# Performance work log

Hardware: AMD Instinct MI355X
Metric: run time of the kernel (lower is better)

## Reference

```python
import jax, jax.numpy as jnp
import numpy as np

B, L = 64, 1024
ENC_DIM, DEC_DIM, ATT_DIM = 512, 512, 512


def setup_inputs() -> dict:
    key = jax.random.key(0)
    ks = jax.random.split(key, 11)
    s_enc = 1.0 / np.sqrt(ENC_DIM)
    s_dec = 1.0 / np.sqrt(DEC_DIM)
    s_att = 1.0 / np.sqrt(ATT_DIM)
    return {
        "encoder_features": jax.random.normal(ks[0], (B, L, ENC_DIM), jnp.float32),
        "decoder_hidden": jax.random.normal(ks[1], (B, DEC_DIM), jnp.float32),
        "coverage": jax.random.uniform(ks[2], (B, L), jnp.float32),
        # nn.Linear params (torch stores weight as [out, in]; we keep [in, out])
        "W_enc": jax.random.uniform(ks[3], (ENC_DIM, ATT_DIM), jnp.float32, -s_enc, s_enc),
        "b_enc": jax.random.uniform(ks[4], (ATT_DIM,), jnp.float32, -s_enc, s_enc),
        "W_dec": jax.random.uniform(ks[5], (DEC_DIM, ATT_DIM), jnp.float32, -s_dec, s_dec),
        "b_dec": jax.random.uniform(ks[6], (ATT_DIM,), jnp.float32, -s_dec, s_dec),
        "W_cov": jax.random.uniform(ks[7], (1, ATT_DIM), jnp.float32, -1.0, 1.0),
        "b_cov": jax.random.uniform(ks[8], (ATT_DIM,), jnp.float32, -1.0, 1.0),
        "W_full": jax.random.uniform(ks[9], (ATT_DIM, 1), jnp.float32, -s_att, s_att),
        "b_full": jax.random.uniform(ks[10], (1,), jnp.float32, -s_att, s_att),
    }


def reference(encoder_features, decoder_hidden, coverage,
              W_enc, b_enc, W_dec, b_dec, W_cov, b_cov, W_full, b_full):
    # att1: [B, L, A]
    att1 = jnp.einsum("ble,ea->bla", encoder_features, W_enc) + b_enc
    # att2: [B, 1, A]
    att2 = (decoder_hidden @ W_dec + b_dec)[:, None, :]
    # att3: coverage[B,L] through Linear(1, A) -> outer product, [B, L, A]
    att3 = coverage[:, :, None] * W_cov[0] + b_cov
    # energy: [B, L]
    energy = (jax.nn.relu(att1 + att2 + att3) @ W_full)[:, :, 0] + b_full[0]
    alpha = jax.nn.softmax(energy, axis=1)  # [B, L]
    new_coverage = coverage + alpha
    attention_weighted_encoding = jnp.einsum("ble,bl->be", encoder_features, alpha)
    return (attention_weighted_encoding, alpha, new_coverage)
```

## Files before the change

kernel.cpp:

```cpp
#include <hip/hip_runtime.h>
#include <cstdint>
#include <cstddef>

#define NB   64
#define NL   1024
#define NA   512
#define NE   512

typedef __attribute__((ext_vector_type(8))) short bf16x8;
typedef __attribute__((ext_vector_type(4))) float f32x4;

__device__ __forceinline__ unsigned short f2bf(float x){
    unsigned int u = __float_as_uint(x);
    u += 0x7FFFu + ((u >> 16) & 1u);
    return (unsigned short)(u >> 16);
}

__global__ __launch_bounds__(256) void k_prep(const float* __restrict__ Wenc,
                                              unsigned short* __restrict__ wfrag,
                                              const float* __restrict__ dh,
                                              const float* __restrict__ Wdec,
                                              const float* __restrict__ bdec,
                                              const float* __restrict__ benc,
                                              const float* __restrict__ bcov,
                                              float* __restrict__ base){
    const int bid = blockIdx.x, tid = threadIdx.x;
    if (bid < 128){
        const int g    = bid * 256 + tid;
        const int lane = g & 63;
        const int n    = (g >> 6) & 3;
        const int ks   = (g >> 8) & 1;
        const int cw   = (g >> 9) & 7;
        const int s    = g >> 12;
        const int col  = cw * 64 + n * 16 + (lane & 15);
        const int kb   = s * 64 + ks * 32 + (lane >> 4) * 8;
        unsigned int w[4];
        #pragma unroll
        for (int p = 0; p < 4; ++p){
            unsigned short lo = f2bf(Wenc[(size_t)(kb + 2*p    ) * NA + col]);
            unsigned short hi = f2bf(Wenc[(size_t)(kb + 2*p + 1) * NA + col]);
            w[p] = (unsigned int)lo | ((unsigned int)hi << 16);
        }
        ((uint4*)wfrag)[g] = make_uint4(w[0], w[1], w[2], w[3]);
    } else {
        const int idx = bid - 128;
        const int b   = idx >> 3;
        const int a0  = (idx & 7) * 64;
        const int al  = tid & 63, kg = tid >> 6;
        __shared__ float h[512];
        __shared__ float ps[4][64];
        h[tid]       = dh[b * 512 + tid];
        h[tid + 256] = dh[b * 512 + tid + 256];
        __syncthreads();
        const float* wp = Wdec + (size_t)(kg * 128) * 512 + a0 + al;
        const float* hp = h + kg * 128;
        float s0 = 0.f, s1 = 0.f, s2 = 0.f, s3 = 0.f;
        #pragma unroll
        for (int k = 0; k < 128; k += 4){
            s0 += hp[k + 0] * wp[(size_t)(k + 0) * 512];
            s1 += hp[k + 1] * wp[(size_t)(k + 1) * 512];
            s2 += hp[k + 2] * wp[(size_t)(k + 2) * 512];
            s3 += hp[k + 3] * wp[(size_t)(k + 3) * 512];
        }
        ps[kg][al] = (s0 + s1) + (s2 + s3);
        __syncthreads();
        if (tid < 64){
            const int a = a0 + tid;
            base[b * 512 + a] = ps[0][tid] + ps[1][tid] + ps[2][tid] + ps[3][tid]
                              + bdec[a] + benc[a] + bcov[a];
        }
    }
}

__global__ __launch_bounds__(256, 2) void k_energy(
        const float* __restrict__ enc,
        const float* __restrict__ cov,
        const float* __restrict__ base,
        const unsigned short* __restrict__ wfrag,
        const float* __restrict__ Wcov,
        const float* __restrict__ Wfull,
        float* __restrict__ energy)
{
    __shared__ __align__(16) unsigned char sB[65536];
    __shared__ __align__(16) unsigned char sA[8192];
    __shared__ float sCov[64];
    __shared__ float sEp[4][64];

    const int tid  = threadIdx.x;
    const int wid  = tid >> 6, lane = tid & 63;
    const int r0   = blockIdx.x * 64;
    const int b    = r0 >> 10;

    if (tid < 64) sCov[tid] = cov[r0 + tid];

    f32x4 acc[4][8];
    #pragma unroll
    for (int m = 0; m < 4; ++m)
        #pragma unroll
        for (int n = 0; n < 8; ++n) acc[m][n] = (f32x4){0.f, 0.f, 0.f, 0.f};

    const int rloc = tid >> 2, q = tid & 3;
    const float* arow = enc + (size_t)(r0 + rloc) * NE + q * 16;
    unsigned char* aw = sA + (((q >> 1) * 4 + (rloc >> 4)) * 1024
                              + ((rloc & 15) + 32 * (q & 1)) * 16);
    const unsigned char* bsrc = (const unsigned char*)wfrag + wid * 16384 + lane * 16;
    unsigned char* bdst = sB + wid * 16384;

    for (int s = 0; s < 8; ++s){
        __syncthreads();
        const unsigned char* bs = bsrc + (size_t)s * 65536;
        #pragma unroll
        for (int i = 0; i < 16; ++i){
            __builtin_amdgcn_global_load_lds(
                (__attribute__((address_space(1))) void*)(bs + i * 1024),
                (__attribute__((address_space(3))) void*)(bdst + i * 1024),
                16, 0, 0);
        }
        const float* ap = arow + s * 64;
        float4 v0 = *(const float4*)(ap);
        float4 v1 = *(const float4*)(ap + 4);
        float4 v2 = *(const float4*)(ap + 8);
        float4 v3 = *(const float4*)(ap + 12);
        uint4 f1, f2;
        f1.x = f2bf(v0.x) | ((unsigned)f2bf(v0.y) << 16);
        f1.y = f2bf(v0.z) | ((unsigned)f2bf(v0.w) << 16);
        f1.z = f2bf(v1.x) | ((unsigned)f2bf(v1.y) << 16);
        f1.w = f2bf(v1.z) | ((unsigned)f2bf(v1.w) << 16);
        f2.x = f2bf(v2.x) | ((unsigned)f2bf(v2.y) << 16);
        f2.y = f2bf(v2.z) | ((unsigned)f2bf(v2.w) << 16);
        f2.z = f2bf(v3.x) | ((unsigned)f2bf(v3.y) << 16);
        f2.w = f2bf(v3.z) | ((unsigned)f2bf(v3.w) << 16);
        *(uint4*)(aw)       = f1;
        *(uint4*)(aw + 256) = f2;
        __syncthreads();
        bf16x8 af[2][4];
        #pragma unroll
        for (int ks = 0; ks < 2; ++ks)
            #pragma unroll
            for (int m = 0; m < 4; ++m)
                af[ks][m] = *(const bf16x8*)(sA + (ks*4 + m) * 1024 + lane * 16);
        #pragma unroll
        for (int ks = 0; ks < 2; ++ks){
            #pragma unroll
            for (int n = 0; n < 8; ++n){
                bf16x8 bfr = *(const bf16x8*)(sB
                    + ((wid*2 + (n>>2)) * 512 + ks * 256 + (n&3) * 64 + lane) * 16);
                #pragma unroll
                for (int m = 0; m < 4; ++m)
                    acc[m][n] = __builtin_amdgcn_mfma_f32_16x16x32_bf16(
                                    af[ks][m], bfr, acc[m][n], 0, 0, 0);
            }
        }
    }

    const int c0 = wid * 128 + (lane & 15);
    float basev[8], wcovv[8], wfullv[8];
    #pragma unroll
    for (int n = 0; n < 8; ++n){
        const int c = c0 + ((n >> 2) * 64) + (n & 3) * 16;
        basev[n]  = base[b * 512 + c];
        wcovv[n]  = Wcov[c];
        wfullv[n] = Wfull[c];
    }
    const int hi = lane >> 4;
    float covr[4][4];
    #pragma unroll
    for (int m = 0; m < 4; ++m)
        #pragma unroll
        for (int r = 0; r < 4; ++r) covr[m][r] = sCov[m*16 + 4*hi + r];
    float epv[4][4] = {};
    #pragma unroll
    for (int m = 0; m < 4; ++m)
        #pragma unroll
        for (int n = 0; n < 8; ++n)
            #pragma unroll
            for (int r = 0; r < 4; ++r){
                float v = acc[m][n][r] + basev[n] + covr[m][r] * wcovv[n];
                v = fmaxf(v, 0.f);
                epv[m][r] += v * wfullv[n];
            }
    #pragma unroll
    for (int m = 0; m < 4; ++m)
        #pragma unroll
        for (int r = 0; r < 4; ++r){
            float v = epv[m][r];
            v += __shfl_xor(v, 1);
            v += __shfl_xor(v, 2);
            v += __shfl_xor(v, 4);
            v += __shfl_xor(v, 8);
            epv[m][r] = v;
        }
    if ((lane & 15) == 0){
        #pragma unroll
        for (int m = 0; m < 4; ++m)
            #pragma unroll
            for (int r = 0; r < 4; ++r)
                sEp[wid][m*16 + 4*hi + r] = epv[m][r];
    }
    __syncthreads();
    if (tid < 64)
        energy[r0 + tid] = sEp[0][tid] + sEp[1][tid] + sEp[2][tid] + sEp[3][tid];
}

#define AWE_OFF   0
#define ALPHA_OFF 32768
#define NCOV_OFF  98304

__global__ __launch_bounds__(256) void k_finish(
        const float* __restrict__ enc, const float* __restrict__ cov,
        const float* __restrict__ energy, float* __restrict__ out)
{
    const int bid = blockIdx.x;
    const int b = bid >> 3, ec = bid & 7;
    const int tid = threadIdx.x;
    __shared__ float sa[1024];
    __shared__ float rb[16];
    __shared__ float ps2[16][64];

    float4 ev = ((const float4*)(energy + b * 1024))[tid];
    float mx = fmaxf(fmaxf(ev.x, ev.y), fmaxf(ev.z, ev.w));
    #pragma unroll
    for (int off = 32; off; off >>= 1) mx = fmaxf(mx, __shfl_xor(mx, off));
    if ((tid & 63) == 0) rb[tid >> 6] = mx;
    __syncthreads();
    mx = fmaxf(fmaxf(rb[0], rb[1]), fmaxf(rb[2], rb[3]));
    float e0 = __expf(ev.x - mx), e1 = __expf(ev.y - mx),
          e2 = __expf(ev.z - mx), e3 = __expf(ev.w - mx);
    ((float4*)sa)[tid] = make_float4(e0, e1, e2, e3);
    float sm = e0 + e1 + e2 + e3;
    #pragma unroll
    for (int off = 32; off; off >>= 1) sm += __shfl_xor(sm, off);
    if ((tid & 63) == 0) rb[8 + (tid >> 6)] = sm;
    __syncthreads();
    const float inv = 1.0f / (rb[8] + rb[9] + rb[10] + rb[11]);

    if (ec == 0){
        #pragma unroll
        for (int i = 0; i < 4; ++i){
            const int idx = tid + i * 256;
            const float a = sa[idx] * inv;
            out[ALPHA_OFF + b * 1024 + idx] = a;
            out[NCOV_OFF  + b * 1024 + idx] = cov[b * 1024 + idx] + a;
        }
    }

    const int cg = tid & 15, rg = tid >> 4;
    const float4* ep = (const float4*)(enc + (size_t)(b * 1024 + rg * 64) * 512)
                     + ec * 16 + cg;
    const float* w = sa + rg * 64;
    float ax = 0.f, ay = 0.f, az = 0.f, aw = 0.f;
    #pragma unroll 8
    for (int l = 0; l < 64; ++l){
        float4 e4 = ep[(size_t)l * 128];
        const float wl = w[l];
        ax += e4.x * wl; ay += e4.y * wl; az += e4.z * wl; aw += e4.w * wl;
    }
    ps2[rg][cg * 4 + 0] = ax;
    ps2[rg][cg * 4 + 1] = ay;
    ps2[rg][cg * 4 + 2] = az;
    ps2[rg][cg * 4 + 3] = aw;
    __syncthreads();
    if (tid < 64){
        float s = 0.f;
        #pragma unroll
        for (int g = 0; g < 16; ++g) s += ps2[g][tid];
        out[AWE_OFF + b * 512 + ec * 64 + tid] = s * inv;
    }
}

extern "C" void kernel_launch(void* const* d_in, const int* in_sizes, int n_in,
                              void* d_out, int out_size, void* d_ws, size_t ws_size,
                              hipStream_t stream){
    const float* enc   = (const float*)d_in[0];
    const float* dh    = (const float*)d_in[1];
    const float* cov   = (const float*)d_in[2];
    const float* Wenc  = (const float*)d_in[3];
    const float* benc  = (const float*)d_in[4];
    const float* Wdec  = (const float*)d_in[5];
    const float* bdec  = (const float*)d_in[6];
    const float* Wcov  = (const float*)d_in[7];
    const float* bcov  = (const float*)d_in[8];
    const float* Wfull = (const float*)d_in[9];
    float* out = (float*)d_out;

    unsigned short* wfrag = (unsigned short*)d_ws;
    float* base   = (float*)((char*)d_ws + 512 * 1024);
    float* energy = (float*)((char*)d_ws + 640 * 1024);

    k_prep  <<<640,  256, 0, stream>>>(Wenc, wfrag, dh, Wdec, bdec, benc, bcov, base);
    k_energy<<<1024, 256, 0, stream>>>(enc, cov, base, wfrag, Wcov, Wfull, energy);
    k_finish<<<512,  256, 0, stream>>>(enc, cov, energy, out);
}
```

Before: 82.07 us.

## Load MFMA operands directly from global memory, dropping LDS staging

The energy GEMM kernel no longer stages the bf16 weight fragments and the converted encoder tile through shared memory. Each wave now reads its B fragments and its fp32 A rows straight from global memory into registers, converting to bf16 in place, which removes the per-step barriers and the 72KB of LDS. The cost is that every wave re-reads the same A rows (four waves share them), and global-load latency now sits directly in front of the MFMAs with no double buffering.

```diff
diff --git a/kernel.cpp b/kernel.cpp
--- a/kernel.cpp
+++ b/kernel.cpp
@@ -9,6 +9,9 @@
 
 typedef __attribute__((ext_vector_type(8))) short bf16x8;
 typedef __attribute__((ext_vector_type(4))) float f32x4;
+typedef __attribute__((ext_vector_type(4))) unsigned int u32x4;
+
+union PackU { u32x4 u; bf16x8 h; };
 
 __device__ __forceinline__ unsigned short f2bf(float x){
     unsigned int u = __float_as_uint(x);
@@ -81,9 +84,6 @@
         const float* __restrict__ Wfull,
         float* __restrict__ energy)
 {
-    __shared__ __align__(16) unsigned char sB[65536];
-    __shared__ __align__(16) unsigned char sA[8192];
-    __shared__ float sCov[64];
     __shared__ float sEp[4][64];
 
     const int tid  = threadIdx.x;
@@ -91,93 +91,72 @@
     const int r0   = blockIdx.x * 64;
     const int b    = r0 >> 10;
 
-    if (tid < 64) sCov[tid] = cov[r0 + tid];
+    const float* aB = enc + (size_t)(r0 + (lane & 15)) * NE + 8 * (lane >> 4);
+    const bf16x8* bB = (const bf16x8*)wfrag + (wid * 2) * 512 + lane;
 
     f32x4 acc[4][8];
     #pragma unroll
     for (int m = 0; m < 4; ++m)
         #pragma unroll
-        for (int n = 0; n < 8; ++n) acc[m][n] = (f32x4){0.f, 0.f, 0.f, 0.f};
-
-    const int rloc = tid >> 2, q = tid & 3;
-    const float* arow = enc + (size_t)(r0 + rloc) * NE + q * 16;
-    unsigned char* aw = sA + (((q >> 1) * 4 + (rloc >> 4)) * 1024
-                              + ((rloc & 15) + 32 * (q & 1)) * 16);
-    const unsigned char* bsrc = (const unsigned char*)wfrag + wid * 16384 + lane * 16;
-    unsigned char* bdst = sB + wid * 16384;
-
+        for (int nn = 0; nn < 8; ++nn) acc[m][nn] = (f32x4){0.f, 0.f, 0.f, 0.f};
+
+    #pragma unroll 1
     for (int s = 0; s < 8; ++s){
-        __syncthreads();
-        const unsigned char* bs = bsrc + (size_t)s * 65536;
-        #pragma unroll
-        for (int i = 0; i < 16; ++i){
-            __builtin_amdgcn_global_load_lds(
-                (__attribute__((address_space(1))) void*)(bs + i * 1024),
-                (__attribute__((address_space(3))) void*)(bdst + i * 1024),
-                16, 0, 0);
-        }
-        const float* ap = arow + s * 64;
-        float4 v0 = *(const float4*)(ap);
-        float4 v1 = *(const float4*)(ap + 4);
-        float4 v2 = *(const float4*)(ap + 8);
-        float4 v3 = *(const float4*)(ap + 12);
-        uint4 f1, f2;
-        f1.x = f2bf(v0.x) | ((unsigned)f2bf(v0.y) << 16);
-        f1.y = f2bf(v0.z) | ((unsigned)f2bf(v0.w) << 16);
-        f1.z = f2bf(v1.x) | ((unsigned)f2bf(v1.y) << 16);
-        f1.w = f2bf(v1.z) | ((unsigned)f2bf(v1.w) << 16);
-        f2.x = f2bf(v2.x) | ((unsigned)f2bf(v2.y) << 16);
-        f2.y = f2bf(v2.z) | ((unsigned)f2bf(v2.w) << 16);
-        f2.z = f2bf(v3.x) | ((unsigned)f2bf(v3.y) << 16);
-        f2.w = f2bf(v3.z) | ((unsigned)f2bf(v3.w) << 16);
-        *(uint4*)(aw)       = f1;
-        *(uint4*)(aw + 256) = f2;
-        __syncthreads();
-        bf16x8 af[2][4];
-        #pragma unroll
-        for (int ks = 0; ks < 2; ++ks)
-            #pragma unroll
-            for (int m = 0; m < 4; ++m)
-                af[ks][m] = *(const bf16x8*)(sA + (ks*4 + m) * 1024 + lane * 16);
         #pragma unroll
         for (int ks = 0; ks < 2; ++ks){
-            #pragma unroll
-            for (int n = 0; n < 8; ++n){
-                bf16x8 bfr = *(const bf16x8*)(sB
-                    + ((wid*2 + (n>>2)) * 512 + ks * 256 + (n&3) * 64 + lane) * 16);
+            bf16x8 bfr[8];
+            #pragma unroll
+            for (int nn = 0; nn < 8; ++nn)
+                bfr[nn] = bB[s * 4096 + (nn >> 2) * 512 + ks * 256 + (nn & 3) * 64];
+            bf16x8 af[4];
+            #pragma unroll
+            for (int m = 0; m < 4; ++m){
+                const float* ap = aB + (size_t)(m * 16) * NE + s * 64 + ks * 32;
+                float4 lo = *(const float4*)(ap);
+                float4 hi = *(const float4*)(ap + 4);
+                PackU u;
+                u.u = (u32x4){
+                    (unsigned)f2bf(lo.x) | ((unsigned)f2bf(lo.y) << 16),
+                    (unsigned)f2bf(lo.z) | ((unsigned)f2bf(lo.w) << 16),
+                    (unsigned)f2bf(hi.x) | ((unsigned)f2bf(hi.y) << 16),
+                    (unsigned)f2bf(hi.z) | ((unsigned)f2bf(hi.w) << 16)};
+                af[m] = u.h;
+            }
+            #pragma unroll
+            for (int nn = 0; nn < 8; ++nn)
                 #pragma unroll
                 for (int m = 0; m < 4; ++m)
-                    acc[m][n] = __builtin_amdgcn_mfma_f32_16x16x32_bf16(
-                                    af[ks][m], bfr, acc[m][n], 0, 0, 0);
-            }
+                    acc[m][nn] = __builtin_amdgcn_mfma_f32_16x16x32_bf16(
+                                    af[m], bfr[nn], acc[m][nn], 0, 0, 0);
         }
     }
 
     const int c0 = wid * 128 + (lane & 15);
     float basev[8], wcovv[8], wfullv[8];
     #pragma unroll
-    for (int n = 0; n < 8; ++n){
-        const int c = c0 + ((n >> 2) * 64) + (n & 3) * 16;
-        basev[n]  = base[b * 512 + c];
-        wcovv[n]  = Wcov[c];
-        wfullv[n] = Wfull[c];
-    }
-    const int hi = lane >> 4;
+    for (int nn = 0; nn < 8; ++nn){
+        const int c = c0 + (nn >> 2) * 64 + (nn & 3) * 16;
+        basev[nn]  = base[b * 512 + c];
+        wcovv[nn]  = Wcov[c];
+        wfullv[nn] = Wfull[c];
+    }
+    const int hi4 = lane >> 4;
     float covr[4][4];
     #pragma unroll
     for (int m = 0; m < 4; ++m)
         #pragma unroll
-        for (int r = 0; r < 4; ++r) covr[m][r] = sCov[m*16 + 4*hi + r];
+        for (int r = 0; r < 4; ++r)
+            covr[m][r] = cov[r0 + m * 16 + 4 * hi4 + r];
     float epv[4][4] = {};
     #pragma unroll
     for (int m = 0; m < 4; ++m)
         #pragma unroll
-        for (int n = 0; n < 8; ++n)
+        for (int nn = 0; nn < 8; ++nn)
             #pragma unroll
             for (int r = 0; r < 4; ++r){
-                float v = acc[m][n][r] + basev[n] + covr[m][r] * wcovv[n];
+                float v = acc[m][nn][r] + basev[nn] + covr[m][r] * wcovv[nn];
                 v = fmaxf(v, 0.f);
-                epv[m][r] += v * wfullv[n];
+                epv[m][r] += v * wfullv[nn];
             }
     #pragma unroll
     for (int m = 0; m < 4; ++m)
@@ -195,7 +174,7 @@
         for (int m = 0; m < 4; ++m)
             #pragma unroll
             for (int r = 0; r < 4; ++r)
-                sEp[wid][m*16 + 4*hi + r] = epv[m][r];
+                sEp[wid][m * 16 + 4 * hi4 + r] = epv[m][r];
     }
     __syncthreads();
     if (tid < 64)
```

After: 127.1 us. 54.8% more time.

## Double-buffer LDS tiles in energy GEMM to overlap loads with MFMA

Applied to the files above, without the earlier changes.

The energy kernel now keeps two LDS buffers each for the bf16 encoder tile and the weight-fragment tile. It prefetches the next K-slice's weights via global_load_lds and holds the raw encoder rows two slices ahead in registers, packing them into the alternate buffer after the MFMA work. This cuts the barriers per K step from two to one and overlaps global latency with compute. In exchange the LDS footprint roughly doubles to about 145KB per block, which likely allows only one block per CU instead of two, and the prefetched encoder rows add register pressure.

```diff
diff --git a/kernel.cpp b/kernel.cpp
--- a/kernel.cpp
+++ b/kernel.cpp
@@ -72,6 +72,25 @@
     }
 }
 
+#define LOAD_RAW(av, ap)                                         \
+    { av[0] = *(const float4*)(ap);                              \
+      av[1] = *(const float4*)((ap) + 4);                        \
+      av[2] = *(const float4*)((ap) + 8);                        \
+      av[3] = *(const float4*)((ap) + 12); }
+
+#define PACK_STORE(av, dst)                                      \
+    { uint4 f1, f2;                                              \
+      f1.x = f2bf(av[0].x) | ((unsigned)f2bf(av[0].y) << 16);    \
+      f1.y = f2bf(av[0].z) | ((unsigned)f2bf(av[0].w) << 16);    \
+      f1.z = f2bf(av[1].x) | ((unsigned)f2bf(av[1].y) << 16);    \
+      f1.w = f2bf(av[1].z) | ((unsigned)f2bf(av[1].w) << 16);    \
+      f2.x = f2bf(av[2].x) | ((unsigned)f2bf(av[2].y) << 16);    \
+      f2.y = f2bf(av[2].z) | ((unsigned)f2bf(av[2].w) << 16);    \
+      f2.z = f2bf(av[3].x) | ((unsigned)f2bf(av[3].y) << 16);    \
+      f2.w = f2bf(av[3].z) | ((unsigned)f2bf(av[3].w) << 16);    \
+      *(uint4*)(dst)       = f1;                                 \
+      *(uint4*)((dst)+256) = f2; }
+
 __global__ __launch_bounds__(256, 2) void k_energy(
         const float* __restrict__ enc,
         const float* __restrict__ cov,
@@ -81,8 +100,8 @@
         const float* __restrict__ Wfull,
         float* __restrict__ energy)
 {
-    __shared__ __align__(16) unsigned char sB[65536];
-    __shared__ __align__(16) unsigned char sA[8192];
+    __shared__ __align__(16) unsigned char sB[2][65536];
+    __shared__ __align__(16) unsigned char sA[2][8192];
     __shared__ float sCov[64];
     __shared__ float sEp[4][64];
 
@@ -101,49 +120,57 @@
 
     const int rloc = tid >> 2, q = tid & 3;
     const float* arow = enc + (size_t)(r0 + rloc) * NE + q * 16;
-    unsigned char* aw = sA + (((q >> 1) * 4 + (rloc >> 4)) * 1024
-                              + ((rloc & 15) + 32 * (q & 1)) * 16);
+    const int awoff = ((q >> 1) * 4 + (rloc >> 4)) * 1024
+                    + ((rloc & 15) + 32 * (q & 1)) * 16;
     const unsigned char* bsrc = (const unsigned char*)wfrag + wid * 16384 + lane * 16;
-    unsigned char* bdst = sB + wid * 16384;
-
-    for (int s = 0; s < 8; ++s){
-        __syncthreads();
-        const unsigned char* bs = bsrc + (size_t)s * 65536;
+
+    float4 avA[4], avB[4];
+
+    {
+        float4 p[4];
+        LOAD_RAW(p, arow);
+        PACK_STORE(p, sA[0] + awoff);
         #pragma unroll
         for (int i = 0; i < 16; ++i){
             __builtin_amdgcn_global_load_lds(
-                (__attribute__((address_space(1))) void*)(bs + i * 1024),
-                (__attribute__((address_space(3))) void*)(bdst + i * 1024),
+                (__attribute__((address_space(1))) void*)(bsrc + i * 1024),
+                (__attribute__((address_space(3))) void*)(sB[0] + wid * 16384 + i * 1024),
                 16, 0, 0);
         }
-        const float* ap = arow + s * 64;
-        float4 v0 = *(const float4*)(ap);
-        float4 v1 = *(const float4*)(ap + 4);
-        float4 v2 = *(const float4*)(ap + 8);
-        float4 v3 = *(const float4*)(ap + 12);
-        uint4 f1, f2;
-        f1.x = f2bf(v0.x) | ((unsigned)f2bf(v0.y) << 16);
-        f1.y = f2bf(v0.z) | ((unsigned)f2bf(v0.w) << 16);
-        f1.z = f2bf(v1.x) | ((unsigned)f2bf(v1.y) << 16);
-        f1.w = f2bf(v1.z) | ((unsigned)f2bf(v1.w) << 16);
-        f2.x = f2bf(v2.x) | ((unsigned)f2bf(v2.y) << 16);
-        f2.y = f2bf(v2.z) | ((unsigned)f2bf(v2.w) << 16);
-        f2.z = f2bf(v3.x) | ((unsigned)f2bf(v3.y) << 16);
-        f2.w = f2bf(v3.z) | ((unsigned)f2bf(v3.w) << 16);
-        *(uint4*)(aw)       = f1;
-        *(uint4*)(aw + 256) = f2;
-        __syncthreads();
+        LOAD_RAW(avB, arow + 64);
+    }
+    __syncthreads();
+
+    #pragma unroll
+    for (int s = 0; s < 8; ++s){
+        const int cb = s & 1;
+        if (s < 6){
+            const float* ap = arow + (s + 2) * 64;
+            if ((s & 1) == 0) { LOAD_RAW(avA, ap) }
+            else              { LOAD_RAW(avB, ap) }
+        }
+        if (s < 7){
+            const unsigned char* bs = bsrc + (size_t)(s + 1) * 65536;
+            unsigned char* bdst = sB[cb ^ 1] + wid * 16384;
+            #pragma unroll
+            for (int i = 0; i < 16; ++i){
+                __builtin_amdgcn_global_load_lds(
+                    (__attribute__((address_space(1))) void*)(bs + i * 1024),
+                    (__attribute__((address_space(3))) void*)(bdst + i * 1024),
+                    16, 0, 0);
+            }
+        }
         bf16x8 af[2][4];
         #pragma unroll
         for (int ks = 0; ks < 2; ++ks)
             #pragma unroll
             for (int m = 0; m < 4; ++m)
-                af[ks][m] = *(const bf16x8*)(sA + (ks*4 + m) * 1024 + lane * 16);
+                af[ks][m] = *(const bf16x8*)(sA[cb] + (ks*4 + m) * 1024 + lane * 16);
         #pragma unroll
         for (int ks = 0; ks < 2; ++ks){
             #pragma unroll
             for (int n = 0; n < 8; ++n){
-                bf16x8 bfr = *(const bf16x8*)(sB
+                bf16x8 bfr = *(const bf16x8*)(sB[cb]
                     + ((wid*2 + (n>>2)) * 512 + ks * 256 + (n&3) * 64 + lane) * 16);
                 #pragma unroll
                 for (int m = 0; m < 4; ++m)
@@ -151,6 +178,11 @@
                                     af[ks][m], bfr, acc[m][n], 0, 0, 0);
             }
         }
+        if (s < 7){
+            if ((s & 1) == 0) { PACK_STORE(avB, sA[cb ^ 1] + awoff) }
+            else              { PACK_STORE(avA, sA[cb ^ 1] + awoff) }
+        }
+        __syncthreads();
     }
 
     const int c0 = wid * 128 + (lane & 15);
```

New measurement: 105.9 us. 29.1% more time.
